# Kernel tuning notes

Measured on AMD Instinct MI355X. Metric: run time of the kernel, lower is better.

Reference implementation:

```python
import jax, jax.numpy as jnp
import numpy as np

B, S, H, I, E, TOP_K, NS = 2, 2048, 2048, 1408, 8, 2, 2
SI = I * NS  # shared expert intermediate (intermediate_size * num_shared_expert)
INIT = 0.02


def setup_inputs() -> dict:
    key = jax.random.key(0)
    ks = jax.random.split(key, 9)
    f32 = jnp.float32
    return {
        "hidden_states": jax.random.normal(ks[0], (B, S, H), f32),
        # router classifier: Linear(H, E, bias=False), torch weight [E, H]
        "router_w": (jax.random.normal(ks[1], (E, H), f32) * INIT),
        # grouped experts (SwiGLU, no bias): [E, H, I], [E, H, I], [E, I, H]
        "gate_w": (jax.random.normal(ks[2], (E, H, I), f32) * INIT),
        "up_w": (jax.random.normal(ks[3], (E, H, I), f32) * INIT),
        "down_w": (jax.random.normal(ks[4], (E, I, H), f32) * INIT),
        # shared expert _MLP (bias=True), stored in matmul orientation
        "s_gate_w": (jax.random.normal(ks[5], (H, SI), f32) * INIT),
        "s_gate_b": jnp.zeros((SI,), f32),
        "s_up_w": (jax.random.normal(ks[6], (H, SI), f32) * INIT),
        "s_up_b": jnp.zeros((SI,), f32),
        "s_down_w": (jax.random.normal(ks[7], (SI, H), f32) * INIT),
        "s_down_b": jnp.zeros((H,), f32),
    }


def reference(hidden_states, router_w, gate_w, up_w, down_w,
              s_gate_w, s_gate_b, s_up_w, s_up_b, s_down_w, s_down_b):
    b, s, h = hidden_states.shape
    x = hidden_states.reshape(-1, h)          # [T, H]
    T = x.shape[0]
    num_experts = router_w.shape[0]

    # ---- router: logits -> fp32 softmax -> top-k -> renormalize ----
    logits = x @ router_w.T                   # [T, E]
    probs = jax.nn.softmax(logits.astype(jnp.float32), axis=-1)
    topk_w, topk_idx = jax.lax.top_k(probs, TOP_K)            # [T, K]
    topk_w = topk_w / jnp.sum(topk_w, axis=-1, keepdims=True)
    # dense combine weights [T, E]; zero for unrouted experts
    combine = jnp.zeros((T, num_experts), probs.dtype)
    combine = combine.at[jnp.arange(T)[:, None], topk_idx].add(topk_w)

    # ---- grouped SwiGLU experts; scan over E keeps peak memory at [T, I] ----
    def expert_step(acc, ws):
        gw, uw, dw, ce = ws                  # [H,I], [H,I], [I,H], [T]
        out = (jax.nn.silu(x @ gw) * (x @ uw)) @ dw           # [T, H]
        return acc + ce[:, None].astype(out.dtype) * out, None

    moe_out, _ = jax.lax.scan(expert_step, jnp.zeros_like(x),
                              (gate_w, up_w, down_w, combine.T))

    # ---- shared expert SwiGLU MLP (bias=True), overlapped -> added ----
    shared = (jax.nn.silu(x @ s_gate_w + s_gate_b)
              * (x @ s_up_w + s_up_b)) @ s_down_w + s_down_b

    return (moe_out + shared).reshape(b, s, h)
```

## Files before the change

kernel.cpp:

```cpp
#include <hip/hip_runtime.h>
#include <hip/hip_bf16.h>
#include <stdint.h>

#define T_TOK 4096
#define HDIM  2048
#define IDIM  1408
#define NEXP  8
#define SIDIM 2816
#define GU_CAP 781
#define DN_CAP 568

typedef __bf16 bf16_t;
typedef __bf16 bf16x8 __attribute__((ext_vector_type(8)));
typedef __bf16 bf16x4 __attribute__((ext_vector_type(4)));
typedef float  f32x4  __attribute__((ext_vector_type(4)));

typedef uint32_t __attribute__((address_space(3))) lds_u32;
typedef uint32_t __attribute__((address_space(1))) glb_u32;

__device__ __forceinline__ void glds16(const bf16_t* g, const char* l) {
  __builtin_amdgcn_global_load_lds((const glb_u32*)g, (lds_u32*)l, 16, 0, 0);
}

__device__ __forceinline__ void bar() {
  asm volatile("" ::: "memory");
  __builtin_amdgcn_s_barrier();
  asm volatile("" ::: "memory");
}
#define VMW4 asm volatile("s_waitcnt vmcnt(4)" ::: "memory")
#define VMW0 asm volatile("s_waitcnt vmcnt(0)" ::: "memory")

__device__ __forceinline__ int xcd_swz(int orig, int nwg) {
  int q = nwg >> 3, r = nwg & 7;
  int x = orig & 7, i = orig >> 3;
  return (x < r ? x * (q + 1) : r * (q + 1) + (x - r) * q) + i;
}

__global__ void tcvt_kernel(const float* __restrict__ in, bf16_t* __restrict__ out, int R, int C) {
  in  += (size_t)blockIdx.z * R * C;
  out += (size_t)blockIdx.z * R * C;
  __shared__ bf16_t tb[64][72];
  const int r0 = blockIdx.y * 64, c0 = blockIdx.x * 64;
  const int tid = threadIdx.x;
  const int cf4 = tid & 15, rr = tid >> 4;
#pragma unroll
  for (int s = 0; s < 4; ++s) {
    int r = rr + 16 * s;
    float4 v = *(const float4*)(in + (size_t)(r0 + r) * C + c0 + cf4 * 4);
    tb[cf4 * 4 + 0][r] = (bf16_t)v.x;
    tb[cf4 * 4 + 1][r] = (bf16_t)v.y;
    tb[cf4 * 4 + 2][r] = (bf16_t)v.z;
    tb[cf4 * 4 + 3][r] = (bf16_t)v.w;
  }
  __syncthreads();
  const int c = tid >> 2, rb = (tid & 3) * 16;
  bf16x8 w0 = *(const bf16x8*)&tb[c][rb];
  bf16x8 w1 = *(const bf16x8*)&tb[c][rb + 8];
  bf16_t* op = out + (size_t)(c0 + c) * R + r0 + rb;
  *(bf16x8*)op = w0;
  *(bf16x8*)(op + 8) = w1;
}

__global__ void tcvt_gu_kernel(const float* __restrict__ in, bf16_t* __restrict__ out,
                               int R, int C, int which) {
  in  += (size_t)blockIdx.z * R * C;
  out += (size_t)blockIdx.z * (2 * C) * R;
  __shared__ bf16_t tb[64][72];
  const int r0 = blockIdx.y * 64, c0 = blockIdx.x * 64;
  const int tid = threadIdx.x;
  const int cf4 = tid & 15, rr = tid >> 4;
#pragma unroll
  for (int s = 0; s < 4; ++s) {
    int r = rr + 16 * s;
    float4 v = *(const float4*)(in + (size_t)(r0 + r) * C + c0 + cf4 * 4);
    tb[cf4 * 4 + 0][r] = (bf16_t)v.x;
    tb[cf4 * 4 + 1][r] = (bf16_t)v.y;
    tb[cf4 * 4 + 2][r] = (bf16_t)v.z;
    tb[cf4 * 4 + 3][r] = (bf16_t)v.w;
  }
  __syncthreads();
  const int c = tid >> 2, rb = (tid & 3) * 16;
  bf16x8 w0 = *(const bf16x8*)&tb[c][rb];
  bf16x8 w1 = *(const bf16x8*)&tb[c][rb + 8];
  int cg = c0 + c;
  int nprime = ((cg >> 4) << 5) + which * 16 + (cg & 15);
  bf16_t* op = out + (size_t)nprime * R + r0 + rb;
  *(bf16x8*)op = w0;
  *(bf16x8*)(op + 8) = w1;
}

__global__ void router_kernel(const float* __restrict__ x, const float* __restrict__ rw,
                              bf16_t* __restrict__ xb,
                              int* __restrict__ tk_i, float* __restrict__ tk_w,
                              int* __restrict__ counts) {
  int gtid = blockIdx.x * 256 + threadIdx.x;
  int t = gtid >> 6, lane = gtid & 63;
  const float4* xr = (const float4*)(x + (size_t)t * HDIM);
  bf16x4* xo = (bf16x4*)(xb + (size_t)t * HDIM);
  float acc[NEXP];
#pragma unroll
  for (int e = 0; e < NEXP; e++) acc[e] = 0.f;
  for (int i = lane; i < HDIM / 4; i += 64) {
    float4 xv = xr[i];
    bf16x4 o;
    o[0] = (bf16_t)xv.x; o[1] = (bf16_t)xv.y; o[2] = (bf16_t)xv.z; o[3] = (bf16_t)xv.w;
    xo[i] = o;
#pragma unroll
    for (int e = 0; e < NEXP; e++) {
      float4 wv = ((const float4*)(rw + e * HDIM))[i];
      acc[e] += xv.x * wv.x + xv.y * wv.y + xv.z * wv.z + xv.w * wv.w;
    }
  }
#pragma unroll
  for (int e = 0; e < NEXP; e++)
#pragma unroll
    for (int off = 32; off; off >>= 1) acc[e] += __shfl_down(acc[e], off);
  if (lane == 0) {
    int i1 = 0; float m1 = acc[0];
#pragma unroll
    for (int e = 1; e < NEXP; e++) if (acc[e] > m1) { m1 = acc[e]; i1 = e; }
    int i2 = -1; float m2 = -1e30f;
#pragma unroll
    for (int e = 0; e < NEXP; e++) if (e != i1 && acc[e] > m2) { m2 = acc[e]; i2 = e; }
    float w1 = 1.f / (1.f + __expf(m2 - m1));
    tk_i[t * 2] = i1; tk_i[t * 2 + 1] = i2;
    tk_w[t * 2] = w1; tk_w[t * 2 + 1] = 1.f - w1;
    atomicAdd(&counts[i1], 1); atomicAdd(&counts[i2], 1);
  }
}

__global__ void build_kernel(int* __restrict__ meta) {
  __shared__ int snmt;
  if (threadIdx.x == 0) {
    int o = 0;
    for (int e = 0; e < NEXP; e++) { meta[16 + e] = o; o += meta[e]; }
    meta[24] = o;
    int nmt = 0;
    for (int e = 0; e < NEXP; e++) {
      int nt = (meta[e] + 255) >> 8;
      for (int i = 0; i < nt; i++) { meta[32 + nmt] = e; meta[80 + nmt] = i << 8; nmt++; }
    }
    meta[25] = nmt;
    meta[26] = nmt * 11 + 352;
    meta[27] = nmt * 8 + 256;
    snmt = nmt;
  }
  __syncthreads();
  const int nmt = snmt;
  int4* gt = (int4*)(meta + 128);
  const int ng = nmt * 11 + 352;
  for (int i = threadIdx.x; i < ng; i += 256) {
    int4 v; v.w = 0;
    if (i < nmt * 11) {
      int g = i / (nmt * 2), rem = i - g * (nmt * 2);
      int yt, xt;
      if (g < 5) { yt = rem >> 1; xt = g * 2 + (rem & 1); }
      else       { yt = rem;      xt = 10; }
      v.x = 0 | (meta[32 + yt] << 1); v.y = meta[80 + yt]; v.z = xt * 256;
    } else {
      int k = i - nmt * 11;
      int g = k >> 5, rem = k & 31;
      int yt = rem >> 1, xt = g * 2 + (rem & 1);
      v.x = 1; v.y = yt * 256; v.z = xt * 256;
    }
    gt[i] = v;
  }
  int4* dt4 = (int4*)(meta + 3328);
  const int nd = nmt * 8 + 256;
  for (int i = threadIdx.x; i < nd; i += 256) {
    int4 v; v.w = 0;
    if (i < nmt * 8) {
      int g = i / (nmt * 2), rem = i - g * (nmt * 2);
      int yt = rem >> 1, xt = g * 2 + (rem & 1);
      v.x = 0 | (meta[32 + yt] << 1); v.y = meta[80 + yt]; v.z = xt * 256;
    } else {
      int k = i - nmt * 8;
      int g = k >> 6, rem = k & 63;
      int inner = rem >> 1, x1 = rem & 1;
      int ks = inner >> 4, yt = inner & 15;
      v.x = 1 | (ks << 4); v.y = yt * 256; v.z = (g * 2 + x1) * 256;
    }
    dt4[i] = v;
  }
}

__global__ void scatter_kernel(const int* __restrict__ tk_i, const float* __restrict__ tk_w,
                               int* __restrict__ meta, int* __restrict__ tok_idx,
                               int* __restrict__ tk_slot) {
  int t = blockIdx.x * 256 + threadIdx.x;
  if (t >= T_TOK) return;
#pragma unroll
  for (int k = 0; k < 2; k++) {
    int e = tk_i[t * 2 + k];
    int pos = meta[16 + e] + atomicAdd(&meta[8 + e], 1);
    tok_idx[pos] = t; tk_slot[t * 2 + k] = pos;
  }
}

template <int OP>
__device__ __forceinline__
void gemm8p_body(const bf16_t* __restrict__ A0, const bf16_t* __restrict__ A1,
                 const bf16_t* __restrict__ B0, const bf16_t* __restrict__ B1,
                 bf16_t* __restrict__ O0, bf16_t* __restrict__ O1, bf16_t* __restrict__ O2,
                 const float* __restrict__ bg, const float* __restrict__ bu,
                 const int* __restrict__ meta, const int* __restrict__ tok_idx) {
  const int ntiles = meta[OP == 0 ? 26 : 27];
  const int l = blockIdx.x;
  if (l >= ntiles) return;
  const int s = xcd_swz(l, ntiles);
  const int4 tv = ((const int4*)(meta + (OP == 0 ? 128 : 3328)))[s];
  const int kind = tv.x & 1, e = (tv.x >> 1) & 7, ks = (tv.x >> 4) & 1;
  const int row0 = tv.y, n0 = tv.z;

  int cnt, slot0 = 0, strideA, strideB, koffA = 0, koffB = 0;
  const bf16_t *Ab, *Bp;
  constexpr int NKT = (OP == 0) ? (HDIM / 64) : (IDIM / 64);
  if (OP == 0) {
    strideA = HDIM; strideB = HDIM; Ab = A0;
    if (kind == 0) {
      slot0 = meta[16 + e]; cnt = meta[17 + e] - slot0;
      Bp = B0 + (size_t)e * (2 * IDIM) * HDIM;
    } else { cnt = T_TOK; Bp = B1; }
  } else {
    if (kind == 0) {
      slot0 = meta[16 + e]; cnt = meta[17 + e] - slot0;
      Ab = A0; strideA = IDIM;
      Bp = B0 + (size_t)e * HDIM * IDIM; strideB = IDIM;
    } else {
      cnt = T_TOK; Ab = A1; strideA = SIDIM; koffA = ks * IDIM;
      Bp = B1; strideB = SIDIM; koffB = ks * IDIM;
    }
  }

  __shared__ __align__(16) char smem[131072];

  const int t = threadIdx.x;
  const int lane = t & 63, wid = t >> 6;
  const int wr = wid >> 2, wc = wid & 3;
  const int lr = lane & 15, lg = lane >> 4;

  const bf16_t* pA[4]; const bf16_t* pB[4]; int dG[4];
#pragma unroll
  for (int j = 0; j < 4; ++j) {
    int g = j * 512 + t;
    int r = g >> 3;
    int c16 = (g & 7) ^ (r & 7);
    dG[j] = g * 16;
    int rr = row0 + r;
    if (kind == 0 && rr >= cnt) rr = cnt - 1;
    int arow;
    if (OP == 0 && kind == 0) arow = tok_idx[slot0 + rr];
    else if (OP == 1 && kind == 0) arow = slot0 + rr;
    else arow = rr;
    pA[j] = Ab + (size_t)arow * strideA + koffA + c16 * 8;
    pB[j] = Bp + (size_t)(n0 + r) * strideB + koffB + c16 * 8;
  }

  const int cswz0 = ((lg) ^ (lr & 7)) * 16;
  const int cswz1 = ((4 + lg) ^ (lr & 7)) * 16;
  const int aRowB = (wr * 128 + lr) * 128;
  const int bRowB = (wc * 64 + lr) * 128 + 65536;

  f32x4 acc[8][4];
#pragma unroll
  for (int mi = 0; mi < 8; ++mi)
#pragma unroll
    for (int ni = 0; ni < 4; ++ni) acc[mi][ni] = (f32x4)(0.f);

  bf16x8 aL[4][2], aH[4][2], bL[2][2], bH[2][2];

#define ST_A(BUFO, KT, JH) { \
    glds16(pA[(JH)*2]   + (KT)*64, smem + (BUFO) + dG[(JH)*2]); \
    glds16(pA[(JH)*2+1] + (KT)*64, smem + (BUFO) + dG[(JH)*2+1]); }
#define ST_B(BUFO, KT, JH) { \
    glds16(pB[(JH)*2]   + (KT)*64, smem + 65536 + (BUFO) + dG[(JH)*2]); \
    glds16(pB[(JH)*2+1] + (KT)*64, smem + 65536 + (BUFO) + dG[(JH)*2+1]); }
#define RD_A(af, BUFO, MIH) { \
    _Pragma("unroll") for (int mi = 0; mi < 4; ++mi) { \
      af[mi][0] = *(const bf16x8*)(smem + (BUFO) + aRowB + (MIH)*8192 + mi*2048 + cswz0); \
      af[mi][1] = *(const bf16x8*)(smem + (BUFO) + aRowB + (MIH)*8192 + mi*2048 + cswz1); } }
#define RD_B(bf, BUFO, NIH) { \
    _Pragma("unroll") for (int ni = 0; ni < 2; ++ni) { \
      bf[ni][0] = *(const bf16x8*)(smem + (BUFO) + bRowB + (NIH)*4096 + ni*2048 + cswz0); \
      bf[ni][1] = *(const bf16x8*)(smem + (BUFO) + bRowB + (NIH)*4096 + ni*2048 + cswz1); } }
#define MMQ(af, bf, MO, NO) { \
    __builtin_amdgcn_s_setprio(1); \
    _Pragma("unroll") for (int ni = 0; ni < 2; ++ni) \
    _Pragma("unroll") for (int mi = 0; mi < 4; ++mi) { \
      acc[(MO)+mi][(NO)+ni] = __builtin_amdgcn_mfma_f32_16x16x32_bf16(af[mi][0], bf[ni][0], acc[(MO)+mi][(NO)+ni], 0, 0, 0); \
      acc[(MO)+mi][(NO)+ni] = __builtin_amdgcn_mfma_f32_16x16x32_bf16(af[mi][1], bf[ni][1], acc[(MO)+mi][(NO)+ni], 0, 0, 0); } \
    __builtin_amdgcn_s_setprio(0); }
#define KTILE(KT, BO, NBO, W) { \
    RD_A(aL, BO, 0); RD_B(bL, BO, 0); \
    if ((KT) + 1 < NKT) ST_B(NBO, (KT) + 1, 0); \
    bar(); MMQ(aL, bL, 0, 0); bar(); \
    RD_A(aH, BO, 1); \
    if ((KT) + 1 < NKT) ST_B(NBO, (KT) + 1, 1); \
    bar(); MMQ(aH, bL, 4, 0); bar(); \
    RD_B(bH, BO, 1); \
    if ((KT) + 2 < NKT) ST_A(BO, (KT) + 2, 0); \
    bar(); MMQ(aH, bH, 4, 2); bar(); \
    if ((KT) + 2 < NKT) ST_A(BO, (KT) + 2, 1); \
    bar(); MMQ(aL, bH, 0, 2); \
    W; bar(); }

  ST_A(0, 0, 0); ST_A(0, 0, 1);
  ST_B(0, 0, 0); ST_B(0, 0, 1);
  ST_A(32768, 1, 0); ST_A(32768, 1, 1);
  VMW4; bar();

  for (int kt = 0; kt < NKT - 2; kt += 2) {
    KTILE(kt, 0, 32768, VMW4);
    KTILE(kt + 1, 32768, 0, VMW4);
  }
  KTILE(NKT - 2, 0, 32768, VMW0);
  KTILE(NKT - 1, 32768, 0, VMW0);

  if (OP == 0) {
    bf16_t* Ho = kind ? O1 : O0;
    const int HN = kind ? SIDIM : IDIM;
    const int Lbase = n0 >> 1;
#pragma unroll
    for (int mi = 0; mi < 8; ++mi)
#pragma unroll
      for (int j = 0; j < 4; ++j) {
        int row = wr * 128 + mi * 16 + lg * 4 + j;
        int grow = row0 + row;
        if (kind == 0 && grow >= cnt) continue;
        size_t orow = (size_t)((kind ? 0 : slot0) + grow);
#pragma unroll
        for (int nih = 0; nih < 2; ++nih) {
          int Lr = wc * 32 + nih * 16 + lr;
          float g = acc[mi][2 * nih][j];
          float u = acc[mi][2 * nih + 1][j];
          if (kind) { g += bg[Lbase + Lr]; u += bu[Lbase + Lr]; }
          float h = (g / (1.f + __expf(-g))) * u;
          Ho[orow * HN + Lbase + Lr] = (bf16_t)h;
        }
      }
  } else {
    bf16_t* Po = kind ? (ks ? O2 : O1) : O0;
#pragma unroll
    for (int mi = 0; mi < 8; ++mi)
#pragma unroll
      for (int j = 0; j < 4; ++j) {
        int row = wr * 128 + mi * 16 + lg * 4 + j;
        int grow = row0 + row;
        if (kind == 0 && grow >= cnt) continue;
        size_t orow = (size_t)((kind ? 0 : slot0) + grow);
#pragma unroll
        for (int ni = 0; ni < 4; ++ni) {
          int col = n0 + wc * 64 + ni * 16 + lr;
          Po[orow * HDIM + col] = (bf16_t)acc[mi][ni][j];
        }
      }
  }
#undef ST_A
#undef ST_B
#undef RD_A
#undef RD_B
#undef MMQ
#undef KTILE
}

__global__ __launch_bounds__(512, 2)
void gu_gemm(const bf16_t* A0, const bf16_t* A1, const bf16_t* B0, const bf16_t* B1,
             bf16_t* O0, bf16_t* O1, bf16_t* O2, const float* bg, const float* bu,
             const int* meta, const int* tok_idx) {
  gemm8p_body<0>(A0, A1, B0, B1, O0, O1, O2, bg, bu, meta, tok_idx);
}
__global__ __launch_bounds__(512, 2)
void dn_gemm(const bf16_t* A0, const bf16_t* A1, const bf16_t* B0, const bf16_t* B1,
             bf16_t* O0, bf16_t* O1, bf16_t* O2, const float* bg, const float* bu,
             const int* meta, const int* tok_idx) {
  gemm8p_body<1>(A0, A1, B0, B1, O0, O1, O2, bg, bu, meta, tok_idx);
}

__global__ void combine_kernel(const bf16_t* __restrict__ sh0, const bf16_t* __restrict__ sh1,
                               const bf16_t* __restrict__ rt, const int* __restrict__ tk_slot,
                               const float* __restrict__ tk_w, const float* __restrict__ sdb,
                               float* __restrict__ out) {
  const int t = blockIdx.x;
  const int c = threadIdx.x * 8;
  const int s1 = tk_slot[2 * t], s2 = tk_slot[2 * t + 1];
  const float w1 = tk_w[2 * t], w2 = tk_w[2 * t + 1];
  bf16x8 a = *(const bf16x8*)(sh0 + (size_t)t * HDIM + c);
  bf16x8 b = *(const bf16x8*)(sh1 + (size_t)t * HDIM + c);
  bf16x8 r1 = *(const bf16x8*)(rt + (size_t)s1 * HDIM + c);
  bf16x8 r2 = *(const bf16x8*)(rt + (size_t)s2 * HDIM + c);
  float4 d0 = *(const float4*)(sdb + c);
  float4 d1 = *(const float4*)(sdb + c + 4);
  float o[8];
#pragma unroll
  for (int i = 0; i < 8; i++)
    o[i] = (float)a[i] + (float)b[i] + w1 * (float)r1[i] + w2 * (float)r2[i];
  o[0] += d0.x; o[1] += d0.y; o[2] += d0.z; o[3] += d0.w;
  o[4] += d1.x; o[5] += d1.y; o[6] += d1.z; o[7] += d1.w;
  float4* op = (float4*)(out + (size_t)t * HDIM + c);
  op[0] = make_float4(o[0], o[1], o[2], o[3]);
  op[1] = make_float4(o[4], o[5], o[6], o[7]);
}

extern "C" void kernel_launch(void* const* d_in, const int* in_sizes, int n_in,
                              void* d_out, int out_size, void* d_ws, size_t ws_size,
                              hipStream_t stream) {
  const float* x_f  = (const float*)d_in[0];
  const float* rw   = (const float*)d_in[1];
  const float* gate = (const float*)d_in[2];
  const float* up   = (const float*)d_in[3];
  const float* down = (const float*)d_in[4];
  const float* sgw  = (const float*)d_in[5];
  const float* sgb  = (const float*)d_in[6];
  const float* suw  = (const float*)d_in[7];
  const float* sub  = (const float*)d_in[8];
  const float* sdw  = (const float*)d_in[9];
  const float* sdb  = (const float*)d_in[10];
  float* out = (float*)d_out;

  char* ws = (char*)d_ws;
  size_t off = 0;
  auto alloc = [&](size_t bytes) {
    char* p = ws + off;
    off += (bytes + 255) & ~(size_t)255;
    return p;
  };
  bf16_t* xb    = (bf16_t*)alloc((size_t)T_TOK * HDIM * 2);
  char*   bgur  = alloc((size_t)NEXP * 2 * IDIM * HDIM * 2);
  bf16_t* BguR  = (bf16_t*)bgur;
  bf16_t* BguS  = (bf16_t*)alloc((size_t)2 * SIDIM * HDIM * 2);
  bf16_t* dT    = (bf16_t*)alloc((size_t)NEXP * HDIM * IDIM * 2);
  bf16_t* sdT   = (bf16_t*)alloc((size_t)HDIM * SIDIM * 2);
  bf16_t* hid_r = (bf16_t*)alloc((size_t)(T_TOK * 2) * IDIM * 2);
  bf16_t* hid_s = (bf16_t*)alloc((size_t)T_TOK * SIDIM * 2);
  int*    meta  = (int*)alloc(32768);
  int*    tok_idx = (int*)alloc(8192 * 4);
  int*    tk_slot = (int*)alloc(8192 * 4);
  int*    tk_i    = (int*)alloc((size_t)T_TOK * 2 * 4);
  float*  tk_w2   = (float*)alloc((size_t)T_TOK * 2 * 4);

  bf16_t* rt_p  = (bf16_t*)bgur;
  bf16_t* sh_p0 = (bf16_t*)(bgur + (size_t)8192 * HDIM * 2);
  bf16_t* sh_p1 = (bf16_t*)(bgur + (size_t)8192 * HDIM * 2 + (size_t)T_TOK * HDIM * 2);

  hipMemsetAsync(meta, 0, 64, stream);

  tcvt_gu_kernel<<<dim3(IDIM / 64, HDIM / 64, NEXP), 256, 0, stream>>>(gate, BguR, HDIM, IDIM, 0);
  tcvt_gu_kernel<<<dim3(IDIM / 64, HDIM / 64, NEXP), 256, 0, stream>>>(up,   BguR, HDIM, IDIM, 1);
  tcvt_gu_kernel<<<dim3(SIDIM / 64, HDIM / 64, 1), 256, 0, stream>>>(sgw, BguS, HDIM, SIDIM, 0);
  tcvt_gu_kernel<<<dim3(SIDIM / 64, HDIM / 64, 1), 256, 0, stream>>>(suw, BguS, HDIM, SIDIM, 1);
  tcvt_kernel<<<dim3(HDIM / 64, IDIM / 64, NEXP), 256, 0, stream>>>(down, dT, IDIM, HDIM);
  tcvt_kernel<<<dim3(HDIM / 64, SIDIM / 64, 1), 256, 0, stream>>>(sdw, sdT, SIDIM, HDIM);

  router_kernel<<<T_TOK / 4, 256, 0, stream>>>(x_f, rw, xb, tk_i, tk_w2, meta);
  build_kernel<<<1, 256, 0, stream>>>(meta);
  scatter_kernel<<<T_TOK / 256, 256, 0, stream>>>(tk_i, tk_w2, meta, tok_idx, tk_slot);

  gu_gemm<<<GU_CAP, 512, 0, stream>>>(
      xb, nullptr, BguR, BguS, hid_r, hid_s, nullptr, sgb, sub, meta, tok_idx);
  dn_gemm<<<DN_CAP, 512, 0, stream>>>(
      hid_r, hid_s, dT, sdT, rt_p, sh_p0, sh_p1, nullptr, nullptr, meta, nullptr);
  combine_kernel<<<T_TOK, 256, 0, stream>>>(sh_p0, sh_p1, rt_p, tk_slot, tk_w2, sdb, out);
}
```

Baseline: 604.5 us.

## Drop split-K for shared down-projection and merge gate/up weight conversion launches

The shared-expert down GEMM previously split K=2816 into two halves, each writing a separate bf16 partial that the combine kernel summed. It now runs the full K loop per tile, which halves the shared tile count and removes one partial buffer read and write. NKT becomes a runtime value, which may hurt unrolling. Separately, the gate and up weight conversion kernels are fused into a single launch per weight group using blockIdx.z. The trade-off is fewer, longer shared tiles, which can reduce parallelism and worsen load balance, in exchange for less memory traffic.

```diff
diff --git a/kernel.cpp b/kernel.cpp
--- a/kernel.cpp
+++ b/kernel.cpp
@@ -8,7 +8,7 @@
 #define NEXP  8
 #define SIDIM 2816
 #define GU_CAP 781
-#define DN_CAP 568
+#define DN_CAP 440
 
 typedef __bf16 bf16_t;
 typedef __bf16 bf16x8 __attribute__((ext_vector_type(8)));
@@ -61,10 +61,11 @@
   *(bf16x8*)(op + 8) = w1;
 }
 
-__global__ void tcvt_gu_kernel(const float* __restrict__ in, bf16_t* __restrict__ out,
-                               int R, int C, int which) {
-  in  += (size_t)blockIdx.z * R * C;
-  out += (size_t)blockIdx.z * (2 * C) * R;
+__global__ void tcvt_gu_kernel(const float* __restrict__ in0, const float* __restrict__ in1,
+                               bf16_t* __restrict__ out, int R, int C) {
+  const int e = blockIdx.z >> 1, which = blockIdx.z & 1;
+  const float* in = (which ? in1 : in0) + (size_t)e * R * C;
+  out += (size_t)e * (2 * C) * R;
   __shared__ bf16_t tb[64][72];
   const int r0 = blockIdx.y * 64, c0 = blockIdx.x * 64;
   const int tid = threadIdx.x;
@@ -142,7 +143,7 @@
     }
     meta[25] = nmt;
     meta[26] = nmt * 11 + 352;
-    meta[27] = nmt * 8 + 256;
+    meta[27] = nmt * 8 + 128;
     snmt = nmt;
   }
   __syncthreads();
@@ -166,7 +167,7 @@
     gt[i] = v;
   }
   int4* dt4 = (int4*)(meta + 3328);
-  const int nd = nmt * 8 + 256;
+  const int nd = nmt * 8 + 128;
   for (int i = threadIdx.x; i < nd; i += 256) {
     int4 v; v.w = 0;
     if (i < nmt * 8) {
@@ -175,10 +176,9 @@
       v.x = 0 | (meta[32 + yt] << 1); v.y = meta[80 + yt]; v.z = xt * 256;
     } else {
       int k = i - nmt * 8;
-      int g = k >> 6, rem = k & 63;
-      int inner = rem >> 1, x1 = rem & 1;
-      int ks = inner >> 4, yt = inner & 15;
-      v.x = 1 | (ks << 4); v.y = yt * 256; v.z = (g * 2 + x1) * 256;
+      int g = k >> 5, rem = k & 31;
+      int yt = rem >> 1, xt = g * 2 + (rem & 1);
+      v.x = 1; v.y = yt * 256; v.z = xt * 256;
     }
     dt4[i] = v;
   }
@@ -201,7 +201,7 @@
 __device__ __forceinline__
 void gemm8p_body(const bf16_t* __restrict__ A0, const bf16_t* __restrict__ A1,
                  const bf16_t* __restrict__ B0, const bf16_t* __restrict__ B1,
-                 bf16_t* __restrict__ O0, bf16_t* __restrict__ O1, bf16_t* __restrict__ O2,
+                 bf16_t* __restrict__ O0, bf16_t* __restrict__ O1,
                  const float* __restrict__ bg, const float* __restrict__ bu,
                  const int* __restrict__ meta, const int* __restrict__ tok_idx) {
   const int ntiles = meta[OP == 0 ? 26 : 27];
@@ -209,13 +209,14 @@
   if (l >= ntiles) return;
   const int s = xcd_swz(l, ntiles);
   const int4 tv = ((const int4*)(meta + (OP == 0 ? 128 : 3328)))[s];
-  const int kind = tv.x & 1, e = (tv.x >> 1) & 7, ks = (tv.x >> 4) & 1;
+  const int kind = tv.x & 1, e = (tv.x >> 1) & 7;
   const int row0 = tv.y, n0 = tv.z;
 
-  int cnt, slot0 = 0, strideA, strideB, koffA = 0, koffB = 0;
+  int cnt, slot0 = 0, strideA, strideB;
   const bf16_t *Ab, *Bp;
-  constexpr int NKT = (OP == 0) ? (HDIM / 64) : (IDIM / 64);
+  int NKT;
   if (OP == 0) {
+    NKT = HDIM / 64;
     strideA = HDIM; strideB = HDIM; Ab = A0;
     if (kind == 0) {
       slot0 = meta[16 + e]; cnt = meta[17 + e] - slot0;
@@ -223,12 +224,14 @@
     } else { cnt = T_TOK; Bp = B1; }
   } else {
     if (kind == 0) {
+      NKT = IDIM / 64;
       slot0 = meta[16 + e]; cnt = meta[17 + e] - slot0;
       Ab = A0; strideA = IDIM;
       Bp = B0 + (size_t)e * HDIM * IDIM; strideB = IDIM;
     } else {
-      cnt = T_TOK; Ab = A1; strideA = SIDIM; koffA = ks * IDIM;
-      Bp = B1; strideB = SIDIM; koffB = ks * IDIM;
+      NKT = SIDIM / 64;
+      cnt = T_TOK; Ab = A1; strideA = SIDIM;
+      Bp = B1; strideB = SIDIM;
     }
   }
 
@@ -252,8 +255,8 @@
     if (OP == 0 && kind == 0) arow = tok_idx[slot0 + rr];
     else if (OP == 1 && kind == 0) arow = slot0 + rr;
     else arow = rr;
-    pA[j] = Ab + (size_t)arow * strideA + koffA + c16 * 8;
-    pB[j] = Bp + (size_t)(n0 + r) * strideB + koffB + c16 * 8;
+    pA[j] = Ab + (size_t)arow * strideA + c16 * 8;
+    pB[j] = Bp + (size_t)(n0 + r) * strideB + c16 * 8;
   }
 
   const int cswz0 = ((lg) ^ (lr & 7)) * 16;
@@ -339,7 +342,7 @@
         }
       }
   } else {
-    bf16_t* Po = kind ? (ks ? O2 : O1) : O0;
+    bf16_t* Po = kind ? O1 : O0;
 #pragma unroll
     for (int mi = 0; mi < 8; ++mi)
 #pragma unroll
@@ -365,18 +368,18 @@
 
 __global__ __launch_bounds__(512, 2)
 void gu_gemm(const bf16_t* A0, const bf16_t* A1, const bf16_t* B0, const bf16_t* B1,
-             bf16_t* O0, bf16_t* O1, bf16_t* O2, const float* bg, const float* bu,
+             bf16_t* O0, bf16_t* O1, const float* bg, const float* bu,
              const int* meta, const int* tok_idx) {
-  gemm8p_body<0>(A0, A1, B0, B1, O0, O1, O2, bg, bu, meta, tok_idx);
+  gemm8p_body<0>(A0, A1, B0, B1, O0, O1, bg, bu, meta, tok_idx);
 }
 __global__ __launch_bounds__(512, 2)
 void dn_gemm(const bf16_t* A0, const bf16_t* A1, const bf16_t* B0, const bf16_t* B1,
-             bf16_t* O0, bf16_t* O1, bf16_t* O2, const float* bg, const float* bu,
+             bf16_t* O0, bf16_t* O1, const float* bg, const float* bu,
              const int* meta, const int* tok_idx) {
-  gemm8p_body<1>(A0, A1, B0, B1, O0, O1, O2, bg, bu, meta, tok_idx);
-}
-
-__global__ void combine_kernel(const bf16_t* __restrict__ sh0, const bf16_t* __restrict__ sh1,
+  gemm8p_body<1>(A0, A1, B0, B1, O0, O1, bg, bu, meta, tok_idx);
+}
+
+__global__ void combine_kernel(const bf16_t* __restrict__ sh,
                                const bf16_t* __restrict__ rt, const int* __restrict__ tk_slot,
                                const float* __restrict__ tk_w, const float* __restrict__ sdb,
                                float* __restrict__ out) {
@@ -384,8 +387,7 @@
   const int c = threadIdx.x * 8;
   const int s1 = tk_slot[2 * t], s2 = tk_slot[2 * t + 1];
   const float w1 = tk_w[2 * t], w2 = tk_w[2 * t + 1];
-  bf16x8 a = *(const bf16x8*)(sh0 + (size_t)t * HDIM + c);
-  bf16x8 b = *(const bf16x8*)(sh1 + (size_t)t * HDIM + c);
+  bf16x8 a = *(const bf16x8*)(sh + (size_t)t * HDIM + c);
   bf16x8 r1 = *(const bf16x8*)(rt + (size_t)s1 * HDIM + c);
   bf16x8 r2 = *(const bf16x8*)(rt + (size_t)s2 * HDIM + c);
   float4 d0 = *(const float4*)(sdb + c);
@@ -393,7 +395,7 @@
   float o[8];
 #pragma unroll
   for (int i = 0; i < 8; i++)
-    o[i] = (float)a[i] + (float)b[i] + w1 * (float)r1[i] + w2 * (float)r2[i];
+    o[i] = (float)a[i] + w1 * (float)r1[i] + w2 * (float)r2[i];
   o[0] += d0.x; o[1] += d0.y; o[2] += d0.z; o[3] += d0.w;
   o[4] += d1.x; o[5] += d1.y; o[6] += d1.z; o[7] += d1.w;
   float4* op = (float4*)(out + (size_t)t * HDIM + c);
@@ -438,16 +440,15 @@
   int*    tk_i    = (int*)alloc((size_t)T_TOK * 2 * 4);
   float*  tk_w2   = (float*)alloc((size_t)T_TOK * 2 * 4);
 
-  bf16_t* rt_p  = (bf16_t*)bgur;
-  bf16_t* sh_p0 = (bf16_t*)(bgur + (size_t)8192 * HDIM * 2);
-  bf16_t* sh_p1 = (bf16_t*)(bgur + (size_t)8192 * HDIM * 2 + (size_t)T_TOK * HDIM * 2);
+  bf16_t* rt_p = (bf16_t*)bgur;
+  bf16_t* sh_p = (bf16_t*)(bgur + (size_t)8192 * HDIM * 2);
 
   hipMemsetAsync(meta, 0, 64, stream);
 
-  tcvt_gu_kernel<<<dim3(IDIM / 64, HDIM / 64, NEXP), 256, 0, stream>>>(gate, BguR, HDIM, IDIM, 0);
-  tcvt_gu_kernel<<<dim3(IDIM / 64, HDIM / 64, NEXP), 256, 0, stream>>>(up,   BguR, HDIM, IDIM, 1);
-  tcvt_gu_kernel<<<dim3(SIDIM / 64, HDIM / 64, 1), 256, 0, stream>>>(sgw, BguS, HDIM, SIDIM, 0);
-  tcvt_gu_kernel<<<dim3(SIDIM / 64, HDIM / 64, 1), 256, 0, stream>>>(suw, BguS, HDIM, SIDIM, 1);
+  tcvt_gu_kernel<<<dim3(IDIM / 64, HDIM / 64, NEXP * 2), 256, 0, stream>>>(
+      gate, up, BguR, HDIM, IDIM);
+  tcvt_gu_kernel<<<dim3(SIDIM / 64, HDIM / 64, 2), 256, 0, stream>>>(
+      sgw, suw, BguS, HDIM, SIDIM);
   tcvt_kernel<<<dim3(HDIM / 64, IDIM / 64, NEXP), 256, 0, stream>>>(down, dT, IDIM, HDIM);
   tcvt_kernel<<<dim3(HDIM / 64, SIDIM / 64, 1), 256, 0, stream>>>(sdw, sdT, SIDIM, HDIM);
 
@@ -456,8 +457,8 @@
   scatter_kernel<<<T_TOK / 256, 256, 0, stream>>>(tk_i, tk_w2, meta, tok_idx, tk_slot);
 
   gu_gemm<<<GU_CAP, 512, 0, stream>>>(
-      xb, nullptr, BguR, BguS, hid_r, hid_s, nullptr, sgb, sub, meta, tok_idx);
+      xb, nullptr, BguR, BguS, hid_r, hid_s, sgb, sub, meta, tok_idx);
   dn_gemm<<<DN_CAP, 512, 0, stream>>>(
-      hid_r, hid_s, dT, sdT, rt_p, sh_p0, sh_p1, nullptr, nullptr, meta, nullptr);
-  combine_kernel<<<T_TOK, 256, 0, stream>>>(sh_p0, sh_p1, rt_p, tk_slot, tk_w2, sdb, out);
-}
+      hid_r, hid_s, dT, sdT, rt_p, sh_p, nullptr, nullptr, meta, nullptr);
+  combine_kernel<<<T_TOK, 256, 0, stream>>>(sh_p, rt_p, tk_slot, tk_w2, sdb, out);
+}
```

Measured after the change: 622.0 us. +2.9%, slower.
